# Kernel tuning notes

Measured on AMD Instinct MI355X. Metric: run time of the kernel, lower is better.

## Reference

```python
import jax, jax.numpy as jnp
import numpy as np


def _binarize_act(z):
    # STE: forward = sign(z), backward = d/dz clamp(z,-1,1)
    clipped = jnp.clip(z, -1.0, 1.0)
    return jax.lax.stop_gradient(jnp.sign(z) - clipped) + clipped


def _binarize_weight(w):
    # per-output-channel scaling factor = mean |w| over (in, kh, kw), detached
    scale = jax.lax.stop_gradient(jnp.mean(jnp.abs(w), axis=(1, 2, 3), keepdims=True))
    clipped = jnp.clip(w, -1.0, 1.0)
    return jax.lax.stop_gradient(scale * jnp.sign(w) - clipped) + clipped


def setup_inputs() -> dict:
    key = jax.random.key(0)
    k = jax.random.split(key, 6)
    B, C, H, W = 16, 64, 256, 256
    return {
        "x": jax.random.normal(k[0], (B, C, H, W), dtype=jnp.float32),
        "move0_bias": jax.random.normal(k[1], (1, C, 1, 1), dtype=jnp.float32) * 0.1,
        "conv_weight": jax.random.normal(k[2], (C, C, 3, 3), dtype=jnp.float32) * 0.1,
        "prelu_weight": jnp.full((C,), 0.25, dtype=jnp.float32)
        + jax.random.normal(k[3], (C,), dtype=jnp.float32) * 0.01,
        "pr_bias0": jax.random.normal(k[4], (1, C, 1, 1), dtype=jnp.float32) * 0.1,
        "pr_bias1": jax.random.normal(k[5], (1, C, 1, 1), dtype=jnp.float32) * 0.1,
    }


def reference(x, move0_bias, conv_weight, prelu_weight, pr_bias0, pr_bias1):
    identity = x  # stride=1, out_channels == in_channels -> no downsample / concat
    z = _binarize_act(x + move0_bias)
    bw = _binarize_weight(conv_weight)
    y = jax.lax.conv_general_dilated(
        z, bw, window_strides=(1, 1), padding=((1, 1), (1, 1)),
        dimension_numbers=("NCHW", "OIHW", "NCHW"))
    # RPReLU: bias0 -> per-channel PReLU -> bias1
    y = y + pr_bias0
    a = prelu_weight.reshape(1, -1, 1, 1)
    y = jnp.where(y > 0, y, a * y)
    y = y + pr_bias1
    return y + identity
```

## Files before the change

kernel.cpp:

```cpp
#include <hip/hip_runtime.h>
#include <stdint.h>

#define Bn 16
#define C 64
#define H 256
#define W 256
#define HW (H * W)
#define NHW (Bn * HW)
#define PPT 4

typedef float f32x4 __attribute__((ext_vector_type(4)));

__global__ void prep_weights(const float* __restrict__ w,
                             uint64_t* __restrict__ wbits,
                             float* __restrict__ scale,
                             int* __restrict__ edgeL,
                             int* __restrict__ edgeR) {
    int o = blockIdx.x;
    int c = threadIdx.x;
    const float* wp = w + ((size_t)o * C + c) * 9;
    float asum = 0.f;
    uint64_t m[9];
#pragma unroll
    for (int tap = 0; tap < 9; ++tap) {
        float v = wp[tap];
        asum += fabsf(v);
        m[tap] = __ballot(v > 0.f);
    }
    if (c == 0) {
#pragma unroll
        for (int tap = 0; tap < 9; ++tap) wbits[o * 9 + tap] = m[tap];
        edgeL[o] = 2 * (int)(__popcll(m[0]) + __popcll(m[3]) + __popcll(m[6]));
        edgeR[o] = 2 * (int)(__popcll(m[2]) + __popcll(m[5]) + __popcll(m[8]));
    }
#pragma unroll
    for (int off = 32; off > 0; off >>= 1)
        asum += __shfl_down(asum, off);
    if (c == 0) scale[o] = asum * (1.f / 576.f);
}

__global__ __launch_bounds__(256) void pack_z(const float* __restrict__ x,
                                              const float* __restrict__ bias,
                                              uint64_t* __restrict__ zbits) {
    int t = blockIdx.x * 256 + threadIdx.x;
    int p0 = t * PPT;
    int n = p0 >> 16;
    int hw = p0 & (HW - 1);
    const float* xp = x + (size_t)n * C * HW + hw;
    uint64_t b0 = 0, b1 = 0, b2 = 0, b3 = 0;
#pragma unroll 8
    for (int c = 0; c < C; ++c) {
        f32x4 v = *reinterpret_cast<const f32x4*>(xp + (size_t)c * HW);
        float bc = bias[c];
        b0 |= (uint64_t)(v.x + bc > 0.f) << c;
        b1 |= (uint64_t)(v.y + bc > 0.f) << c;
        b2 |= (uint64_t)(v.z + bc > 0.f) << c;
        b3 |= (uint64_t)(v.w + bc > 0.f) << c;
    }
    ulonglong2* zp = reinterpret_cast<ulonglong2*>(zbits + p0);
    zp[0] = make_ulonglong2(b0, b1);
    zp[1] = make_ulonglong2(b2, b3);
}

__global__ __launch_bounds__(256) void bconv(const uint64_t* __restrict__ zbits,
                                             const uint64_t* __restrict__ wbits,
                                             const float* __restrict__ scale,
                                             const int* __restrict__ edgeL,
                                             const int* __restrict__ edgeR,
                                             const float* __restrict__ x,
                                             const float* __restrict__ pb0,
                                             const float* __restrict__ aw,
                                             const float* __restrict__ pb1,
                                             float* __restrict__ out) {
    __shared__ uint64_t swb[576];
    __shared__ float sscale[C], spb0[C], sa[C], spb1[C];
    __shared__ int sEL[C], sER[C];
    int t = threadIdx.x;
    if (t < C) {
        sscale[t] = scale[t];
        spb0[t]   = pb0[t];
        sa[t]     = aw[t];
        spb1[t]   = pb1[t];
        sEL[t]    = edgeL[t];
        sER[t]    = edgeR[t];
    }
    for (int i = t; i < 576; i += 256) swb[i] = wbits[i];
    __syncthreads();

    int p0 = (blockIdx.x * 256 + t) * PPT;
    int n  = p0 >> 16;
    int hw = p0 & (HW - 1);
    int h  = hw >> 8;
    int w0 = hw & (W - 1);

    const uint64_t* zr = zbits + (size_t)n * HW;
    uint64_t zb[3][6];
#pragma unroll
    for (int i = 0; i < 3; ++i) {
        int hh = h - 1 + i;
        bool rv = (unsigned)hh < (unsigned)H;
#pragma unroll
        for (int j = 0; j < 6; ++j) {
            int cc = w0 - 1 + j;
            bool cv = (unsigned)cc < (unsigned)W;
            zb[i][j] = (rv && cv) ? zr[hh * W + cc] : 0ull;
        }
    }

    const float* xid = x + (size_t)n * C * HW + hw;
    float* op = out + (size_t)n * C * HW + hw;

    bool leftE  = (w0 == 0);
    bool rightE = (w0 == W - PPT);

    if (h >= 1 && h <= H - 2) {
#pragma unroll 2
        for (int o = 0; o < C; ++o) {
            const uint64_t* wp = &swb[o * 9];
            int s0 = 0, s1 = 0, s2 = 0, s3 = 0;
#pragma unroll
            for (int i = 0; i < 3; ++i)
#pragma unroll
                for (int jj = 0; jj < 3; ++jj) {
                    uint64_t wt = wp[i * 3 + jj];
                    s0 += (int)__popcll(wt ^ zb[i][jj]);
                    s1 += (int)__popcll(wt ^ zb[i][jj + 1]);
                    s2 += (int)__popcll(wt ^ zb[i][jj + 2]);
                    s3 += (int)__popcll(wt ^ zb[i][jj + 3]);
                }
            int d0 = 576 - 2 * s0, d1 = 576 - 2 * s1;
            int d2 = 576 - 2 * s2, d3 = 576 - 2 * s3;
            if (leftE)  d0 += sEL[o] - 192;
            if (rightE) d3 += sER[o] - 192;

            float sc = sscale[o], bb0 = spb0[o], af = sa[o], bb1 = spb1[o];
            f32x4 idv = *reinterpret_cast<const f32x4*>(xid + (size_t)o * HW);
            f32x4 r;
            float y;
            y = sc * (float)d0 + bb0; y = y > 0.f ? y : af * y; r.x = y + bb1 + idv.x;
            y = sc * (float)d1 + bb0; y = y > 0.f ? y : af * y; r.y = y + bb1 + idv.y;
            y = sc * (float)d2 + bb0; y = y > 0.f ? y : af * y; r.z = y + bb1 + idv.z;
            y = sc * (float)d3 + bb0; y = y > 0.f ? y : af * y; r.w = y + bb1 + idv.w;
            __builtin_nontemporal_store(r, reinterpret_cast<f32x4*>(op + (size_t)o * HW));
        }
    } else {
        int vrow[3], vcol[6];
#pragma unroll
        for (int i = 0; i < 3; ++i)
            vrow[i] = ((unsigned)(h - 1 + i) < (unsigned)H) ? -1 : 0;
#pragma unroll
        for (int j = 0; j < 6; ++j)
            vcol[j] = ((unsigned)(w0 - 1 + j) < (unsigned)W) ? -1 : 0;
        int nv[4];
#pragma unroll
        for (int q = 0; q < 4; ++q) {
            int nr = (vrow[0] & 1) + (vrow[1] & 1) + (vrow[2] & 1);
            int nc = (vcol[q] & 1) + (vcol[q + 1] & 1) + (vcol[q + 2] & 1);
            nv[q] = nr * nc;
        }
#pragma unroll 2
        for (int o = 0; o < C; ++o) {
            const uint64_t* wp = &swb[o * 9];
            int s[4] = {0, 0, 0, 0};
#pragma unroll
            for (int i = 0; i < 3; ++i)
#pragma unroll
                for (int jj = 0; jj < 3; ++jj) {
                    uint64_t wt = wp[i * 3 + jj];
#pragma unroll
                    for (int q = 0; q < 4; ++q)
                        s[q] += (vrow[i] & vcol[q + jj]) &
                                (int)__popcll(wt ^ zb[i][q + jj]);
                }
            float sc = sscale[o], bb0 = spb0[o], af = sa[o], bb1 = spb1[o];
            f32x4 idv = *reinterpret_cast<const f32x4*>(xid + (size_t)o * HW);
            f32x4 r;
            float y;
            y = sc * (float)(64 * nv[0] - 2 * s[0]) + bb0; y = y > 0.f ? y : af * y; r.x = y + bb1 + idv.x;
            y = sc * (float)(64 * nv[1] - 2 * s[1]) + bb0; y = y > 0.f ? y : af * y; r.y = y + bb1 + idv.y;
            y = sc * (float)(64 * nv[2] - 2 * s[2]) + bb0; y = y > 0.f ? y : af * y; r.z = y + bb1 + idv.z;
            y = sc * (float)(64 * nv[3] - 2 * s[3]) + bb0; y = y > 0.f ? y : af * y; r.w = y + bb1 + idv.w;
            __builtin_nontemporal_store(r, reinterpret_cast<f32x4*>(op + (size_t)o * HW));
        }
    }
}

extern "C" void kernel_launch(void* const* d_in, const int* in_sizes, int n_in,
                              void* d_out, int out_size, void* d_ws, size_t ws_size,
                              hipStream_t stream) {
    const float* x           = (const float*)d_in[0];
    const float* move0_bias  = (const float*)d_in[1];
    const float* conv_weight = (const float*)d_in[2];
    const float* prelu_w     = (const float*)d_in[3];
    const float* pr_bias0    = (const float*)d_in[4];
    const float* pr_bias1    = (const float*)d_in[5];
    float* out = (float*)d_out;

    uint8_t* ws = (uint8_t*)d_ws;
    uint64_t* zbits = (uint64_t*)ws;
    uint64_t* wbits = (uint64_t*)(ws + (size_t)NHW * 8);
    float* scale    = (float*)(ws + (size_t)NHW * 8 + 576 * 8);
    int* edgeL      = (int*)(ws + (size_t)NHW * 8 + 576 * 8 + 256);
    int* edgeR      = (int*)(ws + (size_t)NHW * 8 + 576 * 8 + 512);

    prep_weights<<<64, 64, 0, stream>>>(conv_weight, wbits, scale, edgeL, edgeR);
    pack_z<<<NHW / PPT / 256, 256, 0, stream>>>(x, move0_bias, zbits);
    bconv<<<NHW / PPT / 256, 256, 0, stream>>>(zbits, wbits, scale, edgeL, edgeR,
                                               x, pr_bias0, prelu_w, pr_bias1, out);
}
```

Baseline: 540.2 us.

## Fuse sign-packing into binary conv using shared-memory tiles with halo

Removes the separate pack_z kernel and its global zbits buffer. Each block now packs a 16x64 tile plus halo of sign bits into shared memory and runs the XNOR-popcount conv from there. The identity loads are software-prefetched two channels ahead, the per-channel parameters are packed into a float4, and the weight rows are padded to stride 10. In exchange the halo is recomputed per tile, so x is read about 1.3x for packing (the halo is 4 columns wide on each side), and the extra shared memory may lower occupancy.

```diff
diff --git a/kernel.cpp b/kernel.cpp
--- a/kernel.cpp
+++ b/kernel.cpp
@@ -7,7 +7,11 @@
 #define W 256
 #define HW (H * W)
 #define NHW (Bn * HW)
-#define PPT 4
+
+#define TW 64
+#define TH 16
+#define SZH 18
+#define SZW 73
 
 typedef float f32x4 __attribute__((ext_vector_type(4)));
 
@@ -39,84 +43,91 @@
     if (c == 0) scale[o] = asum * (1.f / 576.f);
 }
 
-__global__ __launch_bounds__(256) void pack_z(const float* __restrict__ x,
-                                              const float* __restrict__ bias,
-                                              uint64_t* __restrict__ zbits) {
-    int t = blockIdx.x * 256 + threadIdx.x;
-    int p0 = t * PPT;
-    int n = p0 >> 16;
-    int hw = p0 & (HW - 1);
-    const float* xp = x + (size_t)n * C * HW + hw;
-    uint64_t b0 = 0, b1 = 0, b2 = 0, b3 = 0;
-#pragma unroll 8
-    for (int c = 0; c < C; ++c) {
-        f32x4 v = *reinterpret_cast<const f32x4*>(xp + (size_t)c * HW);
-        float bc = bias[c];
-        b0 |= (uint64_t)(v.x + bc > 0.f) << c;
-        b1 |= (uint64_t)(v.y + bc > 0.f) << c;
-        b2 |= (uint64_t)(v.z + bc > 0.f) << c;
-        b3 |= (uint64_t)(v.w + bc > 0.f) << c;
-    }
-    ulonglong2* zp = reinterpret_cast<ulonglong2*>(zbits + p0);
-    zp[0] = make_ulonglong2(b0, b1);
-    zp[1] = make_ulonglong2(b2, b3);
-}
-
-__global__ __launch_bounds__(256) void bconv(const uint64_t* __restrict__ zbits,
-                                             const uint64_t* __restrict__ wbits,
-                                             const float* __restrict__ scale,
-                                             const int* __restrict__ edgeL,
-                                             const int* __restrict__ edgeR,
-                                             const float* __restrict__ x,
-                                             const float* __restrict__ pb0,
-                                             const float* __restrict__ aw,
-                                             const float* __restrict__ pb1,
-                                             float* __restrict__ out) {
-    __shared__ uint64_t swb[576];
-    __shared__ float sscale[C], spb0[C], sa[C], spb1[C];
+__global__ __launch_bounds__(256) void bconv_fused(
+        const uint64_t* __restrict__ wbits,
+        const float* __restrict__ scale,
+        const int* __restrict__ edgeL,
+        const int* __restrict__ edgeR,
+        const float* __restrict__ x,
+        const float* __restrict__ bias,
+        const float* __restrict__ pb0,
+        const float* __restrict__ aw,
+        const float* __restrict__ pb1,
+        float* __restrict__ out) {
+    __shared__ uint64_t swb[640];
+    __shared__ uint64_t sz[SZH * SZW];
+    __shared__ float4 sprm[C];
+    __shared__ float sbias[C];
     __shared__ int sEL[C], sER[C];
+
     int t = threadIdx.x;
     if (t < C) {
-        sscale[t] = scale[t];
-        spb0[t]   = pb0[t];
-        sa[t]     = aw[t];
-        spb1[t]   = pb1[t];
-        sEL[t]    = edgeL[t];
-        sER[t]    = edgeR[t];
-    }
-    for (int i = t; i < 576; i += 256) swb[i] = wbits[i];
+        sprm[t] = make_float4(scale[t], pb0[t], aw[t], pb1[t]);
+        sbias[t] = bias[t];
+        sEL[t] = edgeL[t];
+        sER[t] = edgeR[t];
+    }
+    for (int i = t; i < 576; i += 256) {
+        int o = i / 9;
+        swb[o * 10 + (i - o * 9)] = wbits[i];
+    }
+
+    int bid = blockIdx.x;
+    int n = bid >> 6;
+    int tile = bid & 63;
+    int ty = tile >> 2, tx = tile & 3;
+    int gh0 = ty * TH, gw0 = tx * TW;
+
+    const float* xn = x + (size_t)n * C * HW;
+
     __syncthreads();
 
-    int p0 = (blockIdx.x * 256 + t) * PPT;
-    int n  = p0 >> 16;
-    int hw = p0 & (HW - 1);
-    int h  = hw >> 8;
-    int w0 = hw & (W - 1);
-
-    const uint64_t* zr = zbits + (size_t)n * HW;
+    for (int ci = t; ci < SZH * 18; ci += 256) {
+        int r = ci / 18;
+        int cb = (ci - r * 18) * 4;
+        int gh = gh0 + r - 1;
+        int gwb = gw0 - 4 + cb;
+        uint64_t b0 = 0, b1 = 0, b2 = 0, b3 = 0;
+        if ((unsigned)gh < (unsigned)H && (unsigned)gwb < (unsigned)(W - 3)) {
+            const float* xp = xn + gh * W + gwb;
+#pragma unroll 8
+            for (int ch = 0; ch < C; ++ch) {
+                f32x4 v = *reinterpret_cast<const f32x4*>(xp + (size_t)ch * HW);
+                float bc = sbias[ch];
+                b0 |= (uint64_t)(v.x + bc > 0.f) << ch;
+                b1 |= (uint64_t)(v.y + bc > 0.f) << ch;
+                b2 |= (uint64_t)(v.z + bc > 0.f) << ch;
+                b3 |= (uint64_t)(v.w + bc > 0.f) << ch;
+            }
+        }
+        uint64_t* zp = &sz[r * SZW + cb];
+        zp[0] = b0; zp[1] = b1; zp[2] = b2; zp[3] = b3;
+    }
+    __syncthreads();
+
+    int tr = t >> 4;
+    int tc4 = (t & 15) * 4;
+    int gh = gh0 + tr;
+    int gw = gw0 + tc4;
+
     uint64_t zb[3][6];
 #pragma unroll
-    for (int i = 0; i < 3; ++i) {
-        int hh = h - 1 + i;
-        bool rv = (unsigned)hh < (unsigned)H;
-#pragma unroll
-        for (int j = 0; j < 6; ++j) {
-            int cc = w0 - 1 + j;
-            bool cv = (unsigned)cc < (unsigned)W;
-            zb[i][j] = (rv && cv) ? zr[hh * W + cc] : 0ull;
-        }
-    }
-
-    const float* xid = x + (size_t)n * C * HW + hw;
-    float* op = out + (size_t)n * C * HW + hw;
-
-    bool leftE  = (w0 == 0);
-    bool rightE = (w0 == W - PPT);
-
-    if (h >= 1 && h <= H - 2) {
+    for (int i = 0; i < 3; ++i)
+#pragma unroll
+        for (int j = 0; j < 6; ++j)
+            zb[i][j] = sz[(tr + i) * SZW + tc4 + 3 + j];
+
+    const float* xid = xn + gh * W + gw;
+    float* op = out + (size_t)n * C * HW + gh * W + gw;
+    bool leftE  = (gw == 0);
+    bool rightE = (gw == W - 4);
+
+    if (gh >= 1 && gh <= H - 2) {
+        f32x4 id0 = *reinterpret_cast<const f32x4*>(xid);
+        f32x4 id1 = *reinterpret_cast<const f32x4*>(xid + HW);
 #pragma unroll 2
         for (int o = 0; o < C; ++o) {
-            const uint64_t* wp = &swb[o * 9];
+            const uint64_t* wp = &swb[o * 10];
             int s0 = 0, s1 = 0, s2 = 0, s3 = 0;
 #pragma unroll
             for (int i = 0; i < 3; ++i)
@@ -133,24 +144,27 @@
             if (leftE)  d0 += sEL[o] - 192;
             if (rightE) d3 += sER[o] - 192;
 
-            float sc = sscale[o], bb0 = spb0[o], af = sa[o], bb1 = spb1[o];
-            f32x4 idv = *reinterpret_cast<const f32x4*>(xid + (size_t)o * HW);
+            float4 pr = sprm[o];
+            f32x4 idv = id0;
+            id0 = id1;
+            if (o < C - 2)
+                id1 = *reinterpret_cast<const f32x4*>(xid + (size_t)(o + 2) * HW);
             f32x4 r;
             float y;
-            y = sc * (float)d0 + bb0; y = y > 0.f ? y : af * y; r.x = y + bb1 + idv.x;
-            y = sc * (float)d1 + bb0; y = y > 0.f ? y : af * y; r.y = y + bb1 + idv.y;
-            y = sc * (float)d2 + bb0; y = y > 0.f ? y : af * y; r.z = y + bb1 + idv.z;
-            y = sc * (float)d3 + bb0; y = y > 0.f ? y : af * y; r.w = y + bb1 + idv.w;
+            y = pr.x * (float)d0 + pr.y; y = y > 0.f ? y : pr.z * y; r.x = y + pr.w + idv.x;
+            y = pr.x * (float)d1 + pr.y; y = y > 0.f ? y : pr.z * y; r.y = y + pr.w + idv.y;
+            y = pr.x * (float)d2 + pr.y; y = y > 0.f ? y : pr.z * y; r.z = y + pr.w + idv.z;
+            y = pr.x * (float)d3 + pr.y; y = y > 0.f ? y : pr.z * y; r.w = y + pr.w + idv.w;
             __builtin_nontemporal_store(r, reinterpret_cast<f32x4*>(op + (size_t)o * HW));
         }
     } else {
         int vrow[3], vcol[6];
 #pragma unroll
         for (int i = 0; i < 3; ++i)
-            vrow[i] = ((unsigned)(h - 1 + i) < (unsigned)H) ? -1 : 0;
+            vrow[i] = ((unsigned)(gh - 1 + i) < (unsigned)H) ? -1 : 0;
 #pragma unroll
         for (int j = 0; j < 6; ++j)
-            vcol[j] = ((unsigned)(w0 - 1 + j) < (unsigned)W) ? -1 : 0;
+            vcol[j] = ((unsigned)(gw - 1 + j) < (unsigned)W) ? -1 : 0;
         int nv[4];
 #pragma unroll
         for (int q = 0; q < 4; ++q) {
@@ -160,7 +174,7 @@
         }
 #pragma unroll 2
         for (int o = 0; o < C; ++o) {
-            const uint64_t* wp = &swb[o * 9];
+            const uint64_t* wp = &swb[o * 10];
             int s[4] = {0, 0, 0, 0};
 #pragma unroll
             for (int i = 0; i < 3; ++i)
@@ -172,14 +186,14 @@
                         s[q] += (vrow[i] & vcol[q + jj]) &
                                 (int)__popcll(wt ^ zb[i][q + jj]);
                 }
-            float sc = sscale[o], bb0 = spb0[o], af = sa[o], bb1 = spb1[o];
+            float4 pr = sprm[o];
             f32x4 idv = *reinterpret_cast<const f32x4*>(xid + (size_t)o * HW);
             f32x4 r;
             float y;
-            y = sc * (float)(64 * nv[0] - 2 * s[0]) + bb0; y = y > 0.f ? y : af * y; r.x = y + bb1 + idv.x;
-            y = sc * (float)(64 * nv[1] - 2 * s[1]) + bb0; y = y > 0.f ? y : af * y; r.y = y + bb1 + idv.y;
-            y = sc * (float)(64 * nv[2] - 2 * s[2]) + bb0; y = y > 0.f ? y : af * y; r.z = y + bb1 + idv.z;
-            y = sc * (float)(64 * nv[3] - 2 * s[3]) + bb0; y = y > 0.f ? y : af * y; r.w = y + bb1 + idv.w;
+            y = pr.x * (float)(64 * nv[0] - 2 * s[0]) + pr.y; y = y > 0.f ? y : pr.z * y; r.x = y + pr.w + idv.x;
+            y = pr.x * (float)(64 * nv[1] - 2 * s[1]) + pr.y; y = y > 0.f ? y : pr.z * y; r.y = y + pr.w + idv.y;
+            y = pr.x * (float)(64 * nv[2] - 2 * s[2]) + pr.y; y = y > 0.f ? y : pr.z * y; r.z = y + pr.w + idv.z;
+            y = pr.x * (float)(64 * nv[3] - 2 * s[3]) + pr.y; y = y > 0.f ? y : pr.z * y; r.w = y + pr.w + idv.w;
             __builtin_nontemporal_store(r, reinterpret_cast<f32x4*>(op + (size_t)o * HW));
         }
     }
@@ -197,14 +211,13 @@
     float* out = (float*)d_out;
 
     uint8_t* ws = (uint8_t*)d_ws;
-    uint64_t* zbits = (uint64_t*)ws;
-    uint64_t* wbits = (uint64_t*)(ws + (size_t)NHW * 8);
-    float* scale    = (float*)(ws + (size_t)NHW * 8 + 576 * 8);
-    int* edgeL      = (int*)(ws + (size_t)NHW * 8 + 576 * 8 + 256);
-    int* edgeR      = (int*)(ws + (size_t)NHW * 8 + 576 * 8 + 512);
+    uint64_t* wbits = (uint64_t*)ws;
+    float* scale    = (float*)(ws + 4608);
+    int* edgeL      = (int*)(ws + 4864);
+    int* edgeR      = (int*)(ws + 5120);
 
     prep_weights<<<64, 64, 0, stream>>>(conv_weight, wbits, scale, edgeL, edgeR);
-    pack_z<<<NHW / PPT / 256, 256, 0, stream>>>(x, move0_bias, zbits);
-    bconv<<<NHW / PPT / 256, 256, 0, stream>>>(zbits, wbits, scale, edgeL, edgeR,
-                                               x, pr_bias0, prelu_w, pr_bias1, out);
+    bconv_fused<<<Bn * (H / TH) * (W / TW), 256, 0, stream>>>(
+        wbits, scale, edgeL, edgeR, x, move0_bias,
+        pr_bias0, prelu_w, pr_bias1, out);
 }
```

After: 567.8 us. 5.1% more time.
